# Kernel optimization log

Measured on AMD Instinct MI355X. Metric: run time of the kernel, lower is better.

## Reference

```python
import jax, jax.numpy as jnp
import numpy as np

B, KLEN, QLEN = 4, 512, 64
KDIM = QDIM = ADIM = 512
H = 4
DK = ADIM // H


def setup_inputs() -> dict:
    key = jax.random.key(0)
    ks = jax.random.split(key, 8)
    inp = {}
    inp["key"] = jax.random.normal(ks[0], (B, KLEN, KDIM), jnp.float32)
    inp["query"] = jax.random.normal(ks[1], (B, QLEN, QDIM), jnp.float32)
    inp["mask"] = jax.random.randint(ks[2], (B, QLEN, KLEN), 0, 2, jnp.int32)
    # nn.Linear default init scale ~ 1/sqrt(fan_in)
    inp["w_key_w"] = jax.random.normal(ks[3], (ADIM, KDIM), jnp.float32) / np.sqrt(KDIM)
    inp["w_key_b"] = jnp.zeros((ADIM,), jnp.float32)
    inp["w_query_w"] = jax.random.normal(ks[4], (ADIM, QDIM), jnp.float32) / np.sqrt(QDIM)
    # weight-normed v: weight = g * v / ||v||_row, g initialized to sqrt(1/adim)
    inp["v_v"] = jax.random.normal(ks[5], (H, ADIM), jnp.float32) / np.sqrt(ADIM)
    inp["v_g"] = jnp.full((H, 1), np.sqrt(1.0 / ADIM), jnp.float32)
    inp["r"] = jnp.array([-4.0], jnp.float32)  # init_r
    return inp


def reference(key, query, mask, w_key_w, w_key_b, w_query_w, v_v, v_g, r):
    bs, klen, _ = key.shape
    qlen = query.shape[1]
    # key projection -> [B, H, klen, d_k]
    k = (jnp.einsum('bkd,ad->bka', key, w_key_w) + w_key_b)
    k = k.reshape(bs, klen, H, DK).transpose(0, 2, 1, 3)
    # query projection (no bias) -> [B, H, qlen, d_k]
    q = jnp.einsum('bqd,ad->bqa', query, w_query_w)
    q = q.reshape(bs, qlen, H, DK).transpose(0, 2, 1, 3)
    # additive energy: relu(k + q) over [B, H, qlen, klen, d_k]
    e5 = jax.nn.relu(k[:, :, None, :, :] + q[:, :, :, None, :])
    # weight-normed v linear mixes heads: Wv[n, h, d]
    Wv = (v_g * v_v / jnp.linalg.norm(v_v, axis=1, keepdims=True)).reshape(H, H, DK)
    e = jnp.einsum('bhqkd,nhd->bnqk', e5, Wv)
    e = e + r[0]
    neg_inf = jnp.finfo(e.dtype).min
    m = jnp.broadcast_to(mask[:, None, :, :], e.shape)  # [B, H, qlen, klen]
    e = jnp.where(m == 0, neg_inf, e)
    return e
```

## Files before the change

kernel.cpp:

```cpp
#include <hip/hip_runtime.h>
#include <math.h>

#define KLEN 512
#define QLEN 64
#define ADIM 512
#define BATCH 4
#define NH 4

typedef __attribute__((ext_vector_type(8))) short bf16x8;
typedef __attribute__((ext_vector_type(4))) float f32x4;
typedef _Float16 f16;
typedef __attribute__((ext_vector_type(2))) _Float16 f16x2;

__device__ __forceinline__ f16x2 u2h(unsigned int u) {
  union { unsigned int u; f16x2 h; } v; v.u = u; return v.h;
}

__device__ __forceinline__ short4 pack4(float4 x) {
  union { unsigned int u[2]; short4 s; } o;
  o.u[0] = __builtin_amdgcn_perm(__float_as_uint(x.y), __float_as_uint(x.x), 0x07060302);
  o.u[1] = __builtin_amdgcn_perm(__float_as_uint(x.w), __float_as_uint(x.z), 0x07060302);
  return o.s;
}

__global__ __launch_bounds__(256) void proj_mfma(
    const float* __restrict__ key, const float* __restrict__ query,
    const float* __restrict__ wk, const float* __restrict__ bk,
    const float* __restrict__ wq,
    const float* __restrict__ v_v, const float* __restrict__ v_g,
    f16* __restrict__ Kp, f16* __restrict__ Qp, f16* __restrict__ Wn) {
  __shared__ short At[2][32 * 40];
  __shared__ short Wt[2][32 * 40];

  const int bid = blockIdx.x;
  const int tid = threadIdx.x;

  if (bid == 1152) {
    __shared__ float wred[256];
    for (int h = 0; h < NH; ++h) {
      float v0 = v_v[h * ADIM + tid];
      float v1 = v_v[h * ADIM + tid + 256];
      wred[tid] = v0 * v0 + v1 * v1;
      __syncthreads();
      for (int s2 = 128; s2 > 0; s2 >>= 1) {
        if (tid < s2) wred[tid] += wred[tid + s2];
        __syncthreads();
      }
      float scale = v_g[h] / sqrtf(wred[0]);
      Wn[h * ADIM + tid] = (f16)(v0 * scale);
      Wn[h * ADIM + tid + 256] = (f16)(v1 * scale);
      __syncthreads();
    }
    return;
  }

  const float *A, *W, *bias;
  f16* C;
  int m0, a0;
  if (bid < 1024) {
    A = key; W = wk; bias = bk; C = Kp;
    m0 = (bid >> 4) * 32; a0 = (bid & 15) * 32;
  } else {
    const int t = bid - 1024;
    A = query; W = wq; bias = nullptr; C = Qp;
    m0 = (t >> 4) * 32; a0 = (t & 15) * 32;
  }

  const int wave = tid >> 6;
  const int wr = wave >> 1;
  const int wc = wave & 1;
  const int lane = tid & 63;
  const int lr = lane & 15, hi = lane >> 4;

  const int srow = tid >> 3;
  const int scol = (tid & 7) * 4;

  const float* Arow = &A[(size_t)(m0 + srow) * ADIM + scol];
  const float* Wrow = &W[(size_t)(a0 + srow) * ADIM + scol];

  f32x4 acc = {0.f, 0.f, 0.f, 0.f};

  {
    float4 fa = *(const float4*)&Arow[0];
    float4 fw = *(const float4*)&Wrow[0];
    *(short4*)&At[0][srow * 40 + scol] = pack4(fa);
    *(short4*)&Wt[0][srow * 40 + scol] = pack4(fw);
  }
  __syncthreads();

  for (int c = 0; c < 16; ++c) {
    float4 na, nw;
    if (c < 15) {
      na = *(const float4*)&Arow[(c + 1) * 32];
      nw = *(const float4*)&Wrow[(c + 1) * 32];
    }
    const short* Ab = At[c & 1];
    const short* Wb = Wt[c & 1];
    bf16x8 af = *(const bf16x8*)&Ab[(wr * 16 + lr) * 40 + hi * 8];
    bf16x8 wf = *(const bf16x8*)&Wb[(wc * 16 + lr) * 40 + hi * 8];
    acc = __builtin_amdgcn_mfma_f32_16x16x32_bf16(af, wf, acc, 0, 0, 0);
    if (c < 15) {
      *(short4*)&At[(c + 1) & 1][srow * 40 + scol] = pack4(na);
      *(short4*)&Wt[(c + 1) & 1][srow * 40 + scol] = pack4(nw);
    }
    __syncthreads();
  }

  const int ccol = a0 + wc * 16 + lr;
  const float bv = bias ? bias[ccol] : 0.f;
#pragma unroll
  for (int i = 0; i < 4; ++i) {
    const int crow = m0 + wr * 16 + hi * 4 + i;
    C[(size_t)crow * ADIM + ccol] = (f16)(acc[i] + bv);
  }
}

__global__ __launch_bounds__(256) void energy_kernel(
    const f16* __restrict__ Kp, const f16* __restrict__ Qp,
    const f16* __restrict__ Wn, const int* __restrict__ mask,
    const float* __restrict__ r, float* __restrict__ out) {
  __shared__ f16 Kl[16 * 520];
  __shared__ f16 Ql[16 * 520];
  __shared__ float Red[2][1280];

  const int b = blockIdx.z;
  const int q0 = blockIdx.y * 16;
  const int kl0 = blockIdx.x * 16;
  const int tid = threadIdx.x;
  const int wave = tid >> 6;
  const int lane = tid & 63;
  const int klg = lane & 7;
  const int qg = lane >> 3;

  const float rv = r[0];

  const unsigned short* Kb = (const unsigned short*)(Kp + ((size_t)b * KLEN + kl0) * ADIM);
  const unsigned short* Qb = (const unsigned short*)(Qp + ((size_t)b * QLEN + q0) * ADIM);

  const unsigned int* Wd = (const unsigned int*)Wn;
  uint4 wreg = *(const uint4*)&Wd[(lane >> 4) * 256 + wave * 64 + (lane & 15) * 4];

#pragma unroll
  for (int j = 0; j < 4; ++j) {
    const int u = tid + 256 * j;
    const int row = u >> 6, c8 = (u & 63) * 8;
    *(uint4*)&Kl[row * 520 + c8] = *(const uint4*)&Kb[row * ADIM + c8];
    *(uint4*)&Ql[row * 520 + c8] = *(const uint4*)&Qb[row * ADIM + c8];
  }
  __syncthreads();

  float acc[2][2][4] = {};
  const int abase = wave * 128;

#pragma unroll
  for (int s = 0; s < 16; ++s) {
    const int off = abase + s * 8;
    uint4 ka = *(const uint4*)&Kl[klg * 520 + off];
    uint4 kb = *(const uint4*)&Kl[(klg + 8) * 520 + off];
    uint4 qa = *(const uint4*)&Ql[qg * 520 + off];
    uint4 qb = *(const uint4*)&Ql[(qg + 8) * 520 + off];
    unsigned wdw[4][4];
#pragma unroll
    for (int n = 0; n < 4; ++n) {
      wdw[n][0] = (unsigned)__builtin_amdgcn_readlane((int)wreg.x, n * 16 + s);
      wdw[n][1] = (unsigned)__builtin_amdgcn_readlane((int)wreg.y, n * 16 + s);
      wdw[n][2] = (unsigned)__builtin_amdgcn_readlane((int)wreg.z, n * 16 + s);
      wdw[n][3] = (unsigned)__builtin_amdgcn_readlane((int)wreg.w, n * 16 + s);
    }
    unsigned ks[2][4] = {{ka.x, ka.y, ka.z, ka.w}, {kb.x, kb.y, kb.z, kb.w}};
    unsigned qs[2][4] = {{qa.x, qa.y, qa.z, qa.w}, {qb.x, qb.y, qb.z, qb.w}};
#pragma unroll
    for (int j = 0; j < 4; ++j) {
      const f16x2 wv0 = u2h(wdw[0][j]), wv1 = u2h(wdw[1][j]);
      const f16x2 wv2 = u2h(wdw[2][j]), wv3 = u2h(wdw[3][j]);
#pragma unroll
      for (int ki = 0; ki < 2; ++ki) {
        const f16x2 kv = u2h(ks[ki][j]);
#pragma unroll
        for (int qi = 0; qi < 2; ++qi) {
          f16x2 sum = kv + u2h(qs[qi][j]);
          f16x2 rl = __builtin_elementwise_max(sum, (f16x2)(_Float16)0);
          acc[ki][qi][0] = __builtin_amdgcn_fdot2(rl, wv0, acc[ki][qi][0], false);
          acc[ki][qi][1] = __builtin_amdgcn_fdot2(rl, wv1, acc[ki][qi][1], false);
          acc[ki][qi][2] = __builtin_amdgcn_fdot2(rl, wv2, acc[ki][qi][2], false);
          acc[ki][qi][3] = __builtin_amdgcn_fdot2(rl, wv3, acc[ki][qi][3], false);
        }
      }
    }
  }

  const int half = wave & 1;
  if (wave < 2) {
#pragma unroll
    for (int ki = 0; ki < 2; ++ki)
#pragma unroll
      for (int qi = 0; qi < 2; ++qi) {
        const int cell = (qg + 8 * qi) * 16 + klg + 8 * ki;
#pragma unroll
        for (int n = 0; n < 4; ++n) Red[half][cell * 5 + n] = acc[ki][qi][n];
      }
  }
  __syncthreads();
  if (wave >= 2) {
#pragma unroll
    for (int ki = 0; ki < 2; ++ki)
#pragma unroll
      for (int qi = 0; qi < 2; ++qi) {
        const int cell = (qg + 8 * qi) * 16 + klg + 8 * ki;
#pragma unroll
        for (int n = 0; n < 4; ++n) Red[half][cell * 5 + n] += acc[ki][qi][n];
      }
  }
  __syncthreads();

  const float NEG_BIG = __uint_as_float(0xFF7F0000u);
  const int n = tid >> 6;
  const int q = (tid >> 2) & 15;
  const int klb = (tid & 3) * 4;
  const int4 mv = *(const int4*)&mask[((size_t)b * QLEN + q0 + q) * KLEN + kl0 + klb];
  const int mm[4] = {mv.x, mv.y, mv.z, mv.w};
  float4 o;
  float* op = &o.x;
#pragma unroll
  for (int t = 0; t < 4; ++t) {
    const int cell = q * 16 + klb + t;
    float v = Red[0][cell * 5 + n] + Red[1][cell * 5 + n] + rv;
    op[t] = mm[t] ? v : NEG_BIG;
  }
  *(float4*)&out[(((size_t)b * NH + n) * QLEN + q0 + q) * KLEN + kl0 + klb] = o;
}

extern "C" void kernel_launch(void* const* d_in, const int* in_sizes, int n_in,
                              void* d_out, int out_size, void* d_ws, size_t ws_size,
                              hipStream_t stream) {
  const float* key   = (const float*)d_in[0];
  const float* query = (const float*)d_in[1];
  const int*   mask  = (const int*)d_in[2];
  const float* wk    = (const float*)d_in[3];
  const float* bk    = (const float*)d_in[4];
  const float* wq    = (const float*)d_in[5];
  const float* v_v   = (const float*)d_in[6];
  const float* v_g   = (const float*)d_in[7];
  const float* r     = (const float*)d_in[8];
  float* out = (float*)d_out;

  f16* Kp = (f16*)d_ws;
  f16* Qp = Kp + (size_t)2048 * 512;
  f16* Wn = Qp + (size_t)256 * 512;

  hipLaunchKernelGGL(proj_mfma, dim3(1153), dim3(256), 0, stream,
                     key, query, wk, bk, wq, v_v, v_g, Kp, Qp, Wn);
  hipLaunchKernelGGL(energy_kernel, dim3(32, 4, 4), dim3(256), 0, stream,
                     Kp, Qp, Wn, mask, r, out);
}
```

Measured before the change: 24.29 us.

## Compute additive energy with f16 MFMA instead of fdot2 and LDS reduction

The energy kernel is restructured so each wave forms relu(k+q) fragments in registers and feeds them to a 16x16x32 f16 MFMA against the normalized head-mixing weights, accumulating over the full 512 dimension. This removes the LDS staging of K/Q tiles, the readlane weight broadcasts, the fdot2 VALU loop and the cross-wave LDS reduction with its barriers. K, Q and W fragments are now read straight from global memory, with K and W prefetched one chunk ahead. The trade-off is that only 4 of the 16 B-columns are meaningful, so three quarters of the MFMA output is discarded, and only a quarter of the lanes store results.

After: 27.02 us. 1.11x slower.

```diff
diff --git a/kernel.cpp b/kernel.cpp
--- a/kernel.cpp
+++ b/kernel.cpp
@@ -11,6 +11,7 @@
 typedef __attribute__((ext_vector_type(4))) float f32x4;
 typedef _Float16 f16;
 typedef __attribute__((ext_vector_type(2))) _Float16 f16x2;
+typedef __attribute__((ext_vector_type(8))) _Float16 f16x8;
 
 __device__ __forceinline__ f16x2 u2h(unsigned int u) {
   union { unsigned int u; f16x2 h; } v; v.u = u; return v.h;
@@ -119,115 +120,79 @@
     const f16* __restrict__ Kp, const f16* __restrict__ Qp,
     const f16* __restrict__ Wn, const int* __restrict__ mask,
     const float* __restrict__ r, float* __restrict__ out) {
-  __shared__ f16 Kl[16 * 520];
-  __shared__ f16 Ql[16 * 520];
-  __shared__ float Red[2][1280];
-
   const int b = blockIdx.z;
   const int q0 = blockIdx.y * 16;
   const int kl0 = blockIdx.x * 16;
   const int tid = threadIdx.x;
   const int wave = tid >> 6;
   const int lane = tid & 63;
-  const int klg = lane & 7;
-  const int qg = lane >> 3;
-
+  const int lr = lane & 15, hi = lane >> 4;
+
+  const unsigned short* Kus = (const unsigned short*)Kp;
+  const unsigned short* Qus = (const unsigned short*)Qp;
+  const unsigned short* Wus = (const unsigned short*)Wn;
+
+  const unsigned short* Krow = &Kus[((size_t)(b * KLEN + kl0 + lr)) * ADIM + hi * 8];
+  const unsigned short* Wrow = &Wus[(size_t)(lr & 3) * ADIM + hi * 8];
+  const unsigned short* Qrow = &Qus[((size_t)(b * QLEN + q0 + wave * 4)) * ADIM + hi * 8];
+
+  f32x4 acc0 = {0,0,0,0}, acc1 = {0,0,0,0}, acc2 = {0,0,0,0}, acc3 = {0,0,0,0};
+
+  union H8 { uint4 u; f16x2 h2[4]; f16x8 v; };
+
+  uint4 kf = *(const uint4*)Krow;
+  uint4 wf = *(const uint4*)Wrow;
+
+#pragma unroll
+  for (int c = 0; c < 16; ++c) {
+    uint4 kn, wn;
+    if (c < 15) {
+      kn = *(const uint4*)&Krow[(c + 1) * 32];
+      wn = *(const uint4*)&Wrow[(c + 1) * 32];
+    }
+    uint4 qf0 = *(const uint4*)&Qrow[0 * ADIM + c * 32];
+    uint4 qf1 = *(const uint4*)&Qrow[1 * ADIM + c * 32];
+    uint4 qf2 = *(const uint4*)&Qrow[2 * ADIM + c * 32];
+    uint4 qf3 = *(const uint4*)&Qrow[3 * ADIM + c * 32];
+    H8 w8; w8.u = wf;
+    const f16x2 kz0 = u2h(kf.x), kz1 = u2h(kf.y), kz2 = u2h(kf.z), kz3 = u2h(kf.w);
+    const f16x2 zero = (f16x2)(_Float16)0;
+#define DO_Q(QF, ACC)                                                          \
+    {                                                                          \
+      H8 a;                                                                    \
+      a.h2[0] = __builtin_elementwise_max(kz0 + u2h(QF.x), zero);              \
+      a.h2[1] = __builtin_elementwise_max(kz1 + u2h(QF.y), zero);              \
+      a.h2[2] = __builtin_elementwise_max(kz2 + u2h(QF.z), zero);              \
+      a.h2[3] = __builtin_elementwise_max(kz3 + u2h(QF.w), zero);              \
+      ACC = __builtin_amdgcn_mfma_f32_16x16x32_f16(a.v, w8.v, ACC, 0, 0, 0);   \
+    }
+    DO_Q(qf0, acc0)
+    DO_Q(qf1, acc1)
+    DO_Q(qf2, acc2)
+    DO_Q(qf3, acc3)
+#undef DO_Q
+    kf = kn; wf = wn;
+  }
+
+  const float NEG_BIG = __uint_as_float(0xFF7F0000u);
   const float rv = r[0];
-
-  const unsigned short* Kb = (const unsigned short*)(Kp + ((size_t)b * KLEN + kl0) * ADIM);
-  const unsigned short* Qb = (const unsigned short*)(Qp + ((size_t)b * QLEN + q0) * ADIM);
-
-  const unsigned int* Wd = (const unsigned int*)Wn;
-  uint4 wreg = *(const uint4*)&Wd[(lane >> 4) * 256 + wave * 64 + (lane & 15) * 4];
-
-#pragma unroll
-  for (int j = 0; j < 4; ++j) {
-    const int u = tid + 256 * j;
-    const int row = u >> 6, c8 = (u & 63) * 8;
-    *(uint4*)&Kl[row * 520 + c8] = *(const uint4*)&Kb[row * ADIM + c8];
-    *(uint4*)&Ql[row * 520 + c8] = *(const uint4*)&Qb[row * ADIM + c8];
-  }
-  __syncthreads();
-
-  float acc[2][2][4] = {};
-  const int abase = wave * 128;
-
-#pragma unroll
-  for (int s = 0; s < 16; ++s) {
-    const int off = abase + s * 8;
-    uint4 ka = *(const uint4*)&Kl[klg * 520 + off];
-    uint4 kb = *(const uint4*)&Kl[(klg + 8) * 520 + off];
-    uint4 qa = *(const uint4*)&Ql[qg * 520 + off];
-    uint4 qb = *(const uint4*)&Ql[(qg + 8) * 520 + off];
-    unsigned wdw[4][4];
-#pragma unroll
-    for (int n = 0; n < 4; ++n) {
-      wdw[n][0] = (unsigned)__builtin_amdgcn_readlane((int)wreg.x, n * 16 + s);
-      wdw[n][1] = (unsigned)__builtin_amdgcn_readlane((int)wreg.y, n * 16 + s);
-      wdw[n][2] = (unsigned)__builtin_amdgcn_readlane((int)wreg.z, n * 16 + s);
-      wdw[n][3] = (unsigned)__builtin_amdgcn_readlane((int)wreg.w, n * 16 + s);
-    }
-    unsigned ks[2][4] = {{ka.x, ka.y, ka.z, ka.w}, {kb.x, kb.y, kb.z, kb.w}};
-    unsigned qs[2][4] = {{qa.x, qa.y, qa.z, qa.w}, {qb.x, qb.y, qb.z, qb.w}};
-#pragma unroll
-    for (int j = 0; j < 4; ++j) {
-      const f16x2 wv0 = u2h(wdw[0][j]), wv1 = u2h(wdw[1][j]);
-      const f16x2 wv2 = u2h(wdw[2][j]), wv3 = u2h(wdw[3][j]);
-#pragma unroll
-      for (int ki = 0; ki < 2; ++ki) {
-        const f16x2 kv = u2h(ks[ki][j]);
-#pragma unroll
-        for (int qi = 0; qi < 2; ++qi) {
-          f16x2 sum = kv + u2h(qs[qi][j]);
-          f16x2 rl = __builtin_elementwise_max(sum, (f16x2)(_Float16)0);
-          acc[ki][qi][0] = __builtin_amdgcn_fdot2(rl, wv0, acc[ki][qi][0], false);
-          acc[ki][qi][1] = __builtin_amdgcn_fdot2(rl, wv1, acc[ki][qi][1], false);
-          acc[ki][qi][2] = __builtin_amdgcn_fdot2(rl, wv2, acc[ki][qi][2], false);
-          acc[ki][qi][3] = __builtin_amdgcn_fdot2(rl, wv3, acc[ki][qi][3], false);
-        }
-      }
-    }
-  }
-
-  const int half = wave & 1;
-  if (wave < 2) {
-#pragma unroll
-    for (int ki = 0; ki < 2; ++ki)
-#pragma unroll
-      for (int qi = 0; qi < 2; ++qi) {
-        const int cell = (qg + 8 * qi) * 16 + klg + 8 * ki;
-#pragma unroll
-        for (int n = 0; n < 4; ++n) Red[half][cell * 5 + n] = acc[ki][qi][n];
-      }
-  }
-  __syncthreads();
-  if (wave >= 2) {
-#pragma unroll
-    for (int ki = 0; ki < 2; ++ki)
-#pragma unroll
-      for (int qi = 0; qi < 2; ++qi) {
-        const int cell = (qg + 8 * qi) * 16 + klg + 8 * ki;
-#pragma unroll
-        for (int n = 0; n < 4; ++n) Red[half][cell * 5 + n] += acc[ki][qi][n];
-      }
-  }
-  __syncthreads();
-
-  const float NEG_BIG = __uint_as_float(0xFF7F0000u);
-  const int n = tid >> 6;
-  const int q = (tid >> 2) & 15;
-  const int klb = (tid & 3) * 4;
-  const int4 mv = *(const int4*)&mask[((size_t)b * QLEN + q0 + q) * KLEN + kl0 + klb];
-  const int mm[4] = {mv.x, mv.y, mv.z, mv.w};
-  float4 o;
-  float* op = &o.x;
-#pragma unroll
-  for (int t = 0; t < 4; ++t) {
-    const int cell = q * 16 + klb + t;
-    float v = Red[0][cell * 5 + n] + Red[1][cell * 5 + n] + rv;
-    op[t] = mm[t] ? v : NEG_BIG;
-  }
-  *(float4*)&out[(((size_t)b * NH + n) * QLEN + q0 + q) * KLEN + kl0 + klb] = o;
+  if (lr < 4) {
+    const int n = lr;
+    const int klb = kl0 + hi * 4;
+    f32x4 accs[4] = {acc0, acc1, acc2, acc3};
+#pragma unroll
+    for (int qi = 0; qi < 4; ++qi) {
+      const int q = q0 + wave * 4 + qi;
+      const int4 mv = *(const int4*)&mask[((size_t)b * QLEN + q) * KLEN + klb];
+      const int mm[4] = {mv.x, mv.y, mv.z, mv.w};
+      float4 o;
+      float* op = &o.x;
+#pragma unroll
+      for (int t = 0; t < 4; ++t)
+        op[t] = mm[t] ? accs[qi][t] + rv : NEG_BIG;
+      *(float4*)&out[(((size_t)b * NH + n) * QLEN + q) * KLEN + klb] = o;
+    }
+  }
 }
 
 extern "C" void kernel_launch(void* const* d_in, const int* in_sizes, int n_in,
```
